# Performance work log

Hardware: AMD Instinct MI355X
Metric: run time of the kernel (lower is better)

The kernel has to match this reference:

```python
import jax, jax.numpy as jnp
import numpy as np

NEG_INF = -1e9


def setup_inputs() -> dict:
    key = jax.random.key(0)
    ks = jax.random.split(key, 12)
    B, S, D, H = 32, 2048, 512, 512
    enc_outs = jax.random.normal(ks[0], (B, S, D), dtype=jnp.float32)
    num_sent = jnp.maximum(jax.random.randint(ks[1], (B,), 0, S), 1).astype(jnp.int64)
    s = 1.0 / np.sqrt(H)
    return {
        "enc_outs": enc_outs,
        "num_sent": num_sent,
        "num_pred": 8,
        "init_h": jax.random.normal(ks[2], (1, H), dtype=jnp.float32) * s,
        "init_c": jax.random.normal(ks[3], (1, H), dtype=jnp.float32) * s,
        "init_in": jax.random.normal(ks[4], (D,), dtype=jnp.float32) * s,
        "W_ih": jax.random.uniform(ks[5], (4 * H, D), jnp.float32, -s, s),
        "W_hh": jax.random.uniform(ks[6], (4 * H, H), jnp.float32, -s, s),
        "b_ih": jax.random.uniform(ks[7], (4 * H,), jnp.float32, -s, s),
        "b_hh": jax.random.uniform(ks[8], (4 * H,), jnp.float32, -s, s),
        "attn_Wq": jax.random.uniform(ks[9], (H, D), jnp.float32, -s, s),
        "score_W": jax.random.uniform(ks[10], (1, H), jnp.float32, -s, s),
        "score_b": jax.random.uniform(ks[11], (1,), jnp.float32, -s, s),
    }


def reference(enc_outs, num_sent, num_pred, init_h, init_c, init_in,
              W_ih, W_hh, b_ih, b_hh, attn_Wq, score_W, score_b):
    B, S, D = enc_outs.shape
    H = init_h.shape[1]
    # rep_mask: True where sentence index is valid
    mask = jnp.arange(S)[None, :] < num_sent[:, None]  # [B, S]

    def lstm_cell(x, h, c):
        gates = x @ W_ih.T + b_ih + h @ W_hh.T + b_hh  # [B, 4H]
        i, f, g, o = jnp.split(gates, 4, axis=-1)
        i, f, o = jax.nn.sigmoid(i), jax.nn.sigmoid(f), jax.nn.sigmoid(o)
        c_new = f * c + i * jnp.tanh(g)
        return o * jnp.tanh(c_new), c_new

    h0 = jnp.broadcast_to(init_h[0], (B, H))
    c0 = jnp.broadcast_to(init_c[0], (B, H))
    in0 = jnp.broadcast_to(init_in, (B, D))

    def step(carry, _):
        h, c, lstm_in = carry
        h, c = lstm_cell(lstm_in, h, c)
        # glimpse attention: bilinear score, masked softmax over sentences
        q = h @ attn_Wq  # [B, D]
        logits = jnp.einsum('bd,bsd->bs', q, enc_outs)
        logits = jnp.where(mask, logits, NEG_INF)
        attn = jax.nn.softmax(logits, axis=-1)
        out = jnp.einsum('bs,bsd->bd', attn, enc_outs)  # [B, D]
        score = out @ score_W.T + score_b  # [B, 1]
        return (h, c, out), score

    _, scores = jax.lax.scan(step, (h0, c0, in0), None, length=int(num_pred))
    return scores  # [num_pred, B, 1]
```

## Files before the change

### kernel.cpp

```cpp
#include <hip/hip_runtime.h>
#include <math.h>

#define B    32
#define S    2048
#define D    512
#define H    512
#define NP   8
#define NSL  32
#define HSL  16
#define NBT  8
#define BG   4
#define NCH  8
#define SCHUNK 256

__device__ __forceinline__ float sigmoidf_(float x) {
  return 1.0f / (1.0f + __expf(-x));
}

__global__ __launch_bounds__(256)
void k_init(const float* __restrict__ W_ih, const float* __restrict__ W_hh,
            const float* __restrict__ init_h, const float* __restrict__ init_c,
            const float* __restrict__ init_in, const int* __restrict__ ns_raw,
            float4* __restrict__ Wt4, float* __restrict__ hbuf, float* __restrict__ cbuf,
            float* __restrict__ xin0, int* __restrict__ ns) {
  __shared__ float tbuf[64][65];
  const int blk = blockIdx.x, tid = threadIdx.x;
  const int jt = blk & 31, kt = blk >> 5;
  const int j0 = jt * 64, k0 = kt * 64;
  const int r0 = tid >> 6, cc = tid & 63;
  for (int rr = r0; rr < 64; rr += 4) {
    int j = j0 + rr, k = k0 + cc;
    tbuf[rr][cc] = (k < 512) ? W_ih[(size_t)j * 512 + k]
                             : W_hh[(size_t)j * 512 + (k - 512)];
  }
  __syncthreads();
  #pragma unroll
  for (int i = 0; i < 4; ++i) {
    const int kk4 = r0 * 4 + i;
    Wt4[(size_t)(kt * 16 + kk4) * 2048 + j0 + cc] =
        make_float4(tbuf[cc][kk4 * 4 + 0], tbuf[cc][kk4 * 4 + 1],
                    tbuf[cc][kk4 * 4 + 2], tbuf[cc][kk4 * 4 + 3]);
  }

  int idx = blk * 256 + tid;
  if (idx < B * H) {
    int d = idx & 511;
    hbuf[idx] = init_h[d];
    cbuf[idx] = init_c[d];
    xin0[idx] = init_in[d];
  }
  if (idx == 0) {
    bool is64 = (ns_raw[1] == 0);
    for (int i2 = 0; i2 < B; ++i2) ns[i2] = is64 ? ns_raw[2 * i2] : ns_raw[i2];
  }
}

__global__ __launch_bounds__(512, 1)
void k_step(const float* __restrict__ xin0, const float* __restrict__ bih,
            const float* __restrict__ bhh, const float* __restrict__ Wq,
            const float* __restrict__ scW, const float* __restrict__ scb,
            const float4* __restrict__ Wt4,
            const float* __restrict__ ch_m, const float* __restrict__ ch_l,
            const float* __restrict__ ch_o,
            float* __restrict__ hbuf, float* __restrict__ cbuf,
            float* __restrict__ qpart, float* __restrict__ out, int t) {
  __shared__ float X[BG][1024];
  __shared__ float gacc[8][64][5];
  __shared__ float gl[4][16][BG];
  __shared__ float hl[BG][16];
  __shared__ float sred[8][BG];

  const int tid = threadIdx.x;
  const int sl = blockIdx.x >> 3;
  const int bg = blockIdx.x & 7;
  const int b0 = bg * BG;

  if (t == 0) {
    #pragma unroll
    for (int bl = 0; bl < BG; ++bl)
      X[bl][tid] = xin0[(b0 + bl) * 512 + tid];
  } else {
    const float swd = scW[tid];
    #pragma unroll
    for (int bl = 0; bl < BG; ++bl) {
      const int b = b0 + bl;
      float M = -1e30f;
      #pragma unroll
      for (int c = 0; c < NCH; ++c) M = fmaxf(M, ch_m[b * NCH + c]);
      float e[NCH]; float L = 0.f;
      #pragma unroll
      for (int c = 0; c < NCH; ++c) {
        e[c] = __expf(ch_m[b * NCH + c] - M);
        L += ch_l[b * NCH + c] * e[c];
      }
      float v = 0.f;
      #pragma unroll
      for (int c = 0; c < NCH; ++c)
        v += ch_o[((size_t)(b * NCH + c)) * 512 + tid] * e[c];
      v *= (1.0f / L);
      X[bl][tid] = v;
      float p = v * swd;
      #pragma unroll
      for (int off = 32; off > 0; off >>= 1) p += __shfl_xor(p, off);
      if ((tid & 63) == 0) sred[tid >> 6][bl] = p;
    }
  }
  if (t < NP) {
    const float4* hsrc = (const float4*)(hbuf + (t & 1) * (B * 512));
    int bl = tid >> 7;
    int off = tid & 127;
    float4 hv = hsrc[(b0 + bl) * 128 + off];
    *(float4*)&X[bl][512 + off * 4] = hv;
  }
  __syncthreads();

  if (t >= 1 && tid < BG) {
    float s = 0.f;
    #pragma unroll
    for (int w = 0; w < 8; ++w) s += sred[w][tid];
    if (sl == 0) out[(t - 1) * B + b0 + tid] = s + scb[0];
  }
  if (t >= NP) return;

  {
    const int jloc = tid & 63;
    const int kc = tid >> 6;
    const int gi = jloc >> 4, ho = jloc & 15;
    const int jg = gi * 512 + sl * HSL + ho;
    const int k0c = kc * 128;
    const float4* wp4 = Wt4 + (size_t)(kc * 32) * 2048 + jg;
    float acc[BG] = {0, 0, 0, 0};
    for (int kk4 = 0; kk4 < 32; kk4 += 4) {
      const float4 w0 = wp4[(size_t)(kk4 + 0) * 2048];
      const float4 w1 = wp4[(size_t)(kk4 + 1) * 2048];
      const float4 w2 = wp4[(size_t)(kk4 + 2) * 2048];
      const float4 w3 = wp4[(size_t)(kk4 + 3) * 2048];
      #pragma unroll
      for (int bl = 0; bl < BG; ++bl) {
        const float4 x0 = *(const float4*)&X[bl][k0c + kk4 * 4];
        const float4 x1 = *(const float4*)&X[bl][k0c + kk4 * 4 + 4];
        const float4 x2 = *(const float4*)&X[bl][k0c + kk4 * 4 + 8];
        const float4 x3 = *(const float4*)&X[bl][k0c + kk4 * 4 + 12];
        acc[bl] += w0.x * x0.x + w0.y * x0.y + w0.z * x0.z + w0.w * x0.w
                 + w1.x * x1.x + w1.y * x1.y + w1.z * x1.z + w1.w * x1.w
                 + w2.x * x2.x + w2.y * x2.y + w2.z * x2.z + w2.w * x2.w
                 + w3.x * x3.x + w3.y * x3.y + w3.z * x3.z + w3.w * x3.w;
      }
    }
    #pragma unroll
    for (int bl = 0; bl < BG; ++bl) gacc[kc][jloc][bl] = acc[bl];
  }
  __syncthreads();

  if (tid < 256) {
    const int bl = tid >> 6, jloc = tid & 63;
    const int gi = jloc >> 4, ho = jloc & 15;
    const int jg = gi * 512 + sl * HSL + ho;
    float g = bih[jg] + bhh[jg];
    #pragma unroll
    for (int kc = 0; kc < 8; ++kc) g += gacc[kc][jloc][bl];
    gl[gi][ho][bl] = g;
  }
  __syncthreads();

  if (tid < BG * HSL) {
    const int ho = tid & 15, bl = tid >> 4;
    const int bglob = b0 + bl, hid = sl * HSL + ho;
    float i_ = sigmoidf_(gl[0][ho][bl]);
    float f_ = sigmoidf_(gl[1][ho][bl]);
    float g_ = tanhf(gl[2][ho][bl]);
    float o_ = sigmoidf_(gl[3][ho][bl]);
    float cv = cbuf[bglob * 512 + hid];
    float cn = f_ * cv + i_ * g_;
    cbuf[bglob * 512 + hid] = cn;
    float hv = o_ * tanhf(cn);
    hbuf[((t + 1) & 1) * (B * 512) + bglob * 512 + hid] = hv;
    hl[bl][ho] = hv;
  }
  __syncthreads();

  {
    float w[HSL];
    #pragma unroll
    for (int ho = 0; ho < HSL; ++ho)
      w[ho] = Wq[(size_t)(sl * HSL + ho) * 512 + tid];
    #pragma unroll
    for (int bl = 0; bl < BG; ++bl) {
      float acc = 0.f;
      #pragma unroll
      for (int ho = 0; ho < HSL; ++ho) acc += hl[bl][ho] * w[ho];
      qpart[((size_t)sl * B + b0 + bl) * 512 + tid] = acc;
    }
  }
}

__global__ __launch_bounds__(512, 1)
void k_attn(const float* __restrict__ enc, const float* __restrict__ qpart,
            const int* __restrict__ ns_buf, float* __restrict__ ch_m,
            float* __restrict__ ch_l, float* __restrict__ ch_o) {
  __shared__ float q_lds[512];
  __shared__ float wm[8], wl[8];
  __shared__ float wo[8][512];
  const int b  = blockIdx.x >> 3;
  const int ch = blockIdx.x & 7;
  const int tid = threadIdx.x;
  const int lane = tid & 63;
  const int wv = tid >> 6;

  {
    float s = 0.f;
    #pragma unroll 8
    for (int sl = 0; sl < NSL; ++sl)
      s += qpart[((size_t)sl * B + b) * 512 + tid];
    q_lds[tid] = s;
  }
  __syncthreads();

  const float4 qa  = *(const float4*)&q_lds[lane * 8];
  const float4 qb4 = *(const float4*)&q_lds[lane * 8 + 4];

  const int s0 = ch * SCHUNK;
  const int nsb = ns_buf[b];
  float m = -1e30f, l = 0.f;
  float o0=0,o1=0,o2=0,o3=0,o4=0,o5=0,o6=0,o7=0;

  const int send = min(s0 + SCHUNK, nsb);
  const size_t rowbase = (size_t)b * S;

  int r = s0 + 2 * wv;
  if (r < send) {
    bool has1 = (r + 1 < send);
    const float4* p0 = (const float4*)(enc + (rowbase + r) * 512 + lane * 8);
    const float4* p1 = (const float4*)(enc + (rowbase + (has1 ? r + 1 : r)) * 512 + lane * 8);
    float4 a0 = p0[0], a1 = p0[1];
    float4 c0 = p1[0], c1 = p1[1];
    while (true) {
      const int rn = r + 16;
      const bool hasn = (rn < send);
      float4 na0, na1, nc0, nc1;
      bool nhas1 = false;
      if (hasn) {
        nhas1 = (rn + 1 < send);
        const float4* f0 = (const float4*)(enc + (rowbase + rn) * 512 + lane * 8);
        const float4* f1 = (const float4*)(enc + (rowbase + (nhas1 ? rn + 1 : rn)) * 512 + lane * 8);
        na0 = f0[0]; na1 = f0[1]; nc0 = f1[0]; nc1 = f1[1];
      }
      float d0 = qa.x*a0.x + qa.y*a0.y + qa.z*a0.z + qa.w*a0.w
               + qb4.x*a1.x + qb4.y*a1.y + qb4.z*a1.z + qb4.w*a1.w;
      float d1 = qa.x*c0.x + qa.y*c0.y + qa.z*c0.z + qa.w*c0.w
               + qb4.x*c1.x + qb4.y*c1.y + qb4.z*c1.z + qb4.w*c1.w;
      #pragma unroll
      for (int off = 32; off > 0; off >>= 1) {
        d0 += __shfl_xor(d0, off);
        d1 += __shfl_xor(d1, off);
      }
      if (!has1) d1 = -1e30f;
      float nm = fmaxf(m, fmaxf(d0, d1));
      float sc = __expf(m - nm);
      float w0 = __expf(d0 - nm);
      float w1 = __expf(d1 - nm);
      l = l * sc + w0 + w1;
      o0 = o0*sc + w0*a0.x + w1*c0.x; o1 = o1*sc + w0*a0.y + w1*c0.y;
      o2 = o2*sc + w0*a0.z + w1*c0.z; o3 = o3*sc + w0*a0.w + w1*c0.w;
      o4 = o4*sc + w0*a1.x + w1*c1.x; o5 = o5*sc + w0*a1.y + w1*c1.y;
      o6 = o6*sc + w0*a1.z + w1*c1.z; o7 = o7*sc + w0*a1.w + w1*c1.w;
      m = nm;
      if (!hasn) break;
      r = rn; has1 = nhas1;
      a0 = na0; a1 = na1; c0 = nc0; c1 = nc1;
    }
  }
  if (lane == 0) { wm[wv] = m; wl[wv] = l; }
  float4* wop = (float4*)&wo[wv][lane * 8];
  wop[0] = make_float4(o0, o1, o2, o3);
  wop[1] = make_float4(o4, o5, o6, o7);
  __syncthreads();

  float M = wm[0];
  #pragma unroll
  for (int w = 1; w < 8; ++w) M = fmaxf(M, wm[w]);
  float e[8]; float L = 0.f;
  #pragma unroll
  for (int w = 0; w < 8; ++w) { e[w] = __expf(wm[w] - M); L += wl[w] * e[w]; }
  if (tid == 0) { ch_m[b * NCH + ch] = M; ch_l[b * NCH + ch] = L; }
  float v = 0.f;
  #pragma unroll
  for (int w = 0; w < 8; ++w) v += wo[w][tid] * e[w];
  ch_o[((size_t)(b * NCH + ch)) * 512 + tid] = v;
}

extern "C" void kernel_launch(void* const* d_in, const int* in_sizes, int n_in,
                              void* d_out, int out_size, void* d_ws, size_t ws_size,
                              hipStream_t stream) {
  const float* enc     = (const float*)d_in[0];
  const int*   ns_raw  = (const int*)d_in[1];
  const float* init_h  = (const float*)d_in[3];
  const float* init_c  = (const float*)d_in[4];
  const float* init_in = (const float*)d_in[5];
  const float* W_ih    = (const float*)d_in[6];
  const float* W_hh    = (const float*)d_in[7];
  const float* b_ih    = (const float*)d_in[8];
  const float* b_hh    = (const float*)d_in[9];
  const float* Wq      = (const float*)d_in[10];
  const float* score_W = (const float*)d_in[11];
  const float* score_b = (const float*)d_in[12];
  float* out = (float*)d_out;

  float* ws    = (float*)d_ws;
  float4* Wt4  = (float4*)ws;
  float* hbuf  = ws + 2097152;
  float* cbuf  = ws + 2129920;
  float* xin0  = ws + 2146304;
  float* qpart = ws + 2162688;
  float* ch_m  = ws + 2686976;
  float* ch_l  = ws + 2687232;
  float* ch_o  = ws + 2687488;
  int*   ns    = (int*)(ws + 2818560);

  k_init<<<512, 256, 0, stream>>>(W_ih, W_hh, init_h, init_c, init_in, ns_raw,
                                  Wt4, hbuf, cbuf, xin0, ns);
  for (int t = 0; t < NP; ++t) {
    k_step<<<NSL * NBT, 512, 0, stream>>>(xin0, b_ih, b_hh, Wq, score_W, score_b, Wt4,
                                          ch_m, ch_l, ch_o, hbuf, cbuf, qpart, out, t);
    k_attn<<<B * NCH, 512, 0, stream>>>(enc, qpart, ns, ch_m, ch_l, ch_o);
  }
  k_step<<<NSL * NBT, 512, 0, stream>>>(xin0, b_ih, b_hh, Wq, score_W, score_b, Wt4,
                                        ch_m, ch_l, ch_o, hbuf, cbuf, qpart, out, NP);
}
```

Measured before the change: 286.4 us.

## Balance attention work by splitting sequences into length-proportional chunks

```diff
diff --git a/kernel.cpp b/kernel.cpp
--- a/kernel.cpp
+++ b/kernel.cpp
@@ -10,8 +10,7 @@
 #define HSL  16
 #define NBT  8
 #define BG   4
-#define NCH  8
-#define SCHUNK 256
+#define MAXCH 256
 
 __device__ __forceinline__ float sigmoidf_(float x) {
   return 1.0f / (1.0f + __expf(-x));
@@ -22,7 +21,9 @@
             const float* __restrict__ init_h, const float* __restrict__ init_c,
             const float* __restrict__ init_in, const int* __restrict__ ns_raw,
             float4* __restrict__ Wt4, float* __restrict__ hbuf, float* __restrict__ cbuf,
-            float* __restrict__ xin0, int* __restrict__ ns) {
+            float* __restrict__ xin0, int* __restrict__ ns,
+            int* __restrict__ chunk_tab, int* __restrict__ chunk_base,
+            int* __restrict__ nchunkA, int* __restrict__ rpcA, int* __restrict__ ctot_g) {
   __shared__ float tbuf[64][65];
   const int blk = blockIdx.x, tid = threadIdx.x;
   const int jt = blk & 31, kt = blk >> 5;
@@ -51,7 +52,23 @@
   }
   if (idx == 0) {
     bool is64 = (ns_raw[1] == 0);
-    for (int i2 = 0; i2 < B; ++i2) ns[i2] = is64 ? ns_raw[2 * i2] : ns_raw[i2];
+    int total = 0;
+    for (int i2 = 0; i2 < B; ++i2) {
+      int v = is64 ? ns_raw[2 * i2] : ns_raw[i2];
+      ns[i2] = v; total += v;
+    }
+    int cidx = 0;
+    for (int b2 = 0; b2 < B; ++b2) {
+      int nch = (224 * ns[b2]) / total;
+      if (nch < 1) nch = 1;
+      int rpc = (ns[b2] + nch - 1) / nch;
+      nch = (ns[b2] + rpc - 1) / rpc;
+      chunk_base[b2] = cidx;
+      nchunkA[b2] = nch;
+      rpcA[b2] = rpc;
+      for (int c = 0; c < nch; ++c) chunk_tab[cidx++] = (b2 << 16) | c;
+    }
+    ctot_g[0] = cidx;
   }
 }
 
@@ -62,6 +79,7 @@
             const float4* __restrict__ Wt4,
             const float* __restrict__ ch_m, const float* __restrict__ ch_l,
             const float* __restrict__ ch_o,
+            const int* __restrict__ chunk_base, const int* __restrict__ nchunkA,
             float* __restrict__ hbuf, float* __restrict__ cbuf,
             float* __restrict__ qpart, float* __restrict__ out, int t) {
   __shared__ float X[BG][1024];
@@ -84,19 +102,15 @@
     #pragma unroll
     for (int bl = 0; bl < BG; ++bl) {
       const int b = b0 + bl;
+      const int cb = chunk_base[b], nc = nchunkA[b];
       float M = -1e30f;
-      #pragma unroll
-      for (int c = 0; c < NCH; ++c) M = fmaxf(M, ch_m[b * NCH + c]);
-      float e[NCH]; float L = 0.f;
-      #pragma unroll
-      for (int c = 0; c < NCH; ++c) {
-        e[c] = __expf(ch_m[b * NCH + c] - M);
-        L += ch_l[b * NCH + c] * e[c];
+      for (int c = 0; c < nc; ++c) M = fmaxf(M, ch_m[cb + c]);
+      float L = 0.f, v = 0.f;
+      for (int c = 0; c < nc; ++c) {
+        float e = __expf(ch_m[cb + c] - M);
+        L += ch_l[cb + c] * e;
+        v += ch_o[((size_t)(cb + c)) * 512 + tid] * e;
       }
-      float v = 0.f;
-      #pragma unroll
-      for (int c = 0; c < NCH; ++c)
-        v += ch_o[((size_t)(b * NCH + c)) * 512 + tid] * e[c];
       v *= (1.0f / L);
       X[bl][tid] = v;
       float p = v * swd;
@@ -196,97 +210,104 @@
 
 __global__ __launch_bounds__(512, 1)
 void k_attn(const float* __restrict__ enc, const float* __restrict__ qpart,
-            const int* __restrict__ ns_buf, float* __restrict__ ch_m,
-            float* __restrict__ ch_l, float* __restrict__ ch_o) {
+            const int* __restrict__ ns_buf, const int* __restrict__ chunk_tab,
+            const int* __restrict__ rpcA, const int* __restrict__ ctot_g,
+            float* __restrict__ ch_m, float* __restrict__ ch_l,
+            float* __restrict__ ch_o) {
   __shared__ float q_lds[512];
   __shared__ float wm[8], wl[8];
   __shared__ float wo[8][512];
-  const int b  = blockIdx.x >> 3;
-  const int ch = blockIdx.x & 7;
   const int tid = threadIdx.x;
   const int lane = tid & 63;
   const int wv = tid >> 6;
-
-  {
-    float s = 0.f;
-    #pragma unroll 8
-    for (int sl = 0; sl < NSL; ++sl)
-      s += qpart[((size_t)sl * B + b) * 512 + tid];
-    q_lds[tid] = s;
-  }
-  __syncthreads();
-
-  const float4 qa  = *(const float4*)&q_lds[lane * 8];
-  const float4 qb4 = *(const float4*)&q_lds[lane * 8 + 4];
-
-  const int s0 = ch * SCHUNK;
-  const int nsb = ns_buf[b];
-  float m = -1e30f, l = 0.f;
-  float o0=0,o1=0,o2=0,o3=0,o4=0,o5=0,o6=0,o7=0;
-
-  const int send = min(s0 + SCHUNK, nsb);
-  const size_t rowbase = (size_t)b * S;
-
-  int r = s0 + 2 * wv;
-  if (r < send) {
-    bool has1 = (r + 1 < send);
-    const float4* p0 = (const float4*)(enc + (rowbase + r) * 512 + lane * 8);
-    const float4* p1 = (const float4*)(enc + (rowbase + (has1 ? r + 1 : r)) * 512 + lane * 8);
-    float4 a0 = p0[0], a1 = p0[1];
-    float4 c0 = p1[0], c1 = p1[1];
-    while (true) {
-      const int rn = r + 16;
-      const bool hasn = (rn < send);
-      float4 na0, na1, nc0, nc1;
-      bool nhas1 = false;
-      if (hasn) {
-        nhas1 = (rn + 1 < send);
-        const float4* f0 = (const float4*)(enc + (rowbase + rn) * 512 + lane * 8);
-        const float4* f1 = (const float4*)(enc + (rowbase + (nhas1 ? rn + 1 : rn)) * 512 + lane * 8);
-        na0 = f0[0]; na1 = f0[1]; nc0 = f1[0]; nc1 = f1[1];
+  const int ctot = ctot_g[0];
+
+  for (int ci = blockIdx.x; ci < ctot; ci += 256) {
+    const int ent = chunk_tab[ci];
+    const int b = ent >> 16, c = ent & 0xffff;
+    const int rpc = rpcA[b];
+    const int s0 = c * rpc;
+    const int send = min(s0 + rpc, ns_buf[b]);
+
+    __syncthreads();
+
+    {
+      float s = 0.f;
+      #pragma unroll 8
+      for (int sl = 0; sl < NSL; ++sl)
+        s += qpart[((size_t)sl * B + b) * 512 + tid];
+      q_lds[tid] = s;
+    }
+    __syncthreads();
+
+    const float4 qa  = *(const float4*)&q_lds[lane * 8];
+    const float4 qb4 = *(const float4*)&q_lds[lane * 8 + 4];
+
+    float m = -1e30f, l = 0.f;
+    float o0=0,o1=0,o2=0,o3=0,o4=0,o5=0,o6=0,o7=0;
+    const size_t rowbase = (size_t)b * S;
+
+    int r = s0 + 2 * wv;
+    if (r < send) {
+      bool has1 = (r + 1 < send);
+      const float4* p0 = (const float4*)(enc + (rowbase + r) * 512 + lane * 8);
+      const float4* p1 = (const float4*)(enc + (rowbase + (has1 ? r + 1 : r)) * 512 + lane * 8);
+      float4 a0 = p0[0], a1 = p0[1];
+      float4 c0 = p1[0], c1 = p1[1];
+      while (true) {
+        const int rn = r + 16;
+        const bool hasn = (rn < send);
+        float4 na0, na1, nc0, nc1;
+        bool nhas1 = false;
+        if (hasn) {
+          nhas1 = (rn + 1 < send);
+          const float4* f0 = (const float4*)(enc + (rowbase + rn) * 512 + lane * 8);
+          const float4* f1 = (const float4*)(enc + (rowbase + (nhas1 ? rn + 1 : rn)) * 512 + lane * 8);
+          na0 = f0[0]; na1 = f0[1]; nc0 = f1[0]; nc1 = f1[1];
+        }
+        float d0 = qa.x*a0.x + qa.y*a0.y + qa.z*a0.z + qa.w*a0.w
+                 + qb4.x*a1.x + qb4.y*a1.y + qb4.z*a1.z + qb4.w*a1.w;
+        float d1 = qa.x*c0.x + qa.y*c0.y + qa.z*c0.z + qa.w*c0.w
+                 + qb4.x*c1.x + qb4.y*c1.y + qb4.z*c1.z + qb4.w*c1.w;
+        #pragma unroll
+        for (int off = 32; off > 0; off >>= 1) {
+          d0 += __shfl_xor(d0, off);
+          d1 += __shfl_xor(d1, off);
+        }
+        if (!has1) d1 = -1e30f;
+        float nm = fmaxf(m, fmaxf(d0, d1));
+        float sc = __expf(m - nm);
+        float w0 = __expf(d0 - nm);
+        float w1 = __expf(d1 - nm);
+        l = l * sc + w0 + w1;
+        o0 = o0*sc + w0*a0.x + w1*c0.x; o1 = o1*sc + w0*a0.y + w1*c0.y;
+        o2 = o2*sc + w0*a0.z + w1*c0.z; o3 = o3*sc + w0*a0.w + w1*c0.w;
+        o4 = o4*sc + w0*a1.x + w1*c1.x; o5 = o5*sc + w0*a1.y + w1*c1.y;
+        o6 = o6*sc + w0*a1.z + w1*c1.z; o7 = o7*sc + w0*a1.w + w1*c1.w;
+        m = nm;
+        if (!hasn) break;
+        r = rn; has1 = nhas1;
+        a0 = na0; a1 = na1; c0 = nc0; c1 = nc1;
       }
-      float d0 = qa.x*a0.x + qa.y*a0.y + qa.z*a0.z + qa.w*a0.w
-               + qb4.x*a1.x + qb4.y*a1.y + qb4.z*a1.z + qb4.w*a1.w;
-      float d1 = qa.x*c0.x + qa.y*c0.y + qa.z*c0.z + qa.w*c0.w
-               + qb4.x*c1.x + qb4.y*c1.y + qb4.z*c1.z + qb4.w*c1.w;
-      #pragma unroll
-      for (int off = 32; off > 0; off >>= 1) {
-        d0 += __shfl_xor(d0, off);
-        d1 += __shfl_xor(d1, off);
-      }
-      if (!has1) d1 = -1e30f;
-      float nm = fmaxf(m, fmaxf(d0, d1));
-      float sc = __expf(m - nm);
-      float w0 = __expf(d0 - nm);
-      float w1 = __expf(d1 - nm);
-      l = l * sc + w0 + w1;
-      o0 = o0*sc + w0*a0.x + w1*c0.x; o1 = o1*sc + w0*a0.y + w1*c0.y;
-      o2 = o2*sc + w0*a0.z + w1*c0.z; o3 = o3*sc + w0*a0.w + w1*c0.w;
-      o4 = o4*sc + w0*a1.x + w1*c1.x; o5 = o5*sc + w0*a1.y + w1*c1.y;
-      o6 = o6*sc + w0*a1.z + w1*c1.z; o7 = o7*sc + w0*a1.w + w1*c1.w;
-      m = nm;
-      if (!hasn) break;
-      r = rn; has1 = nhas1;
-      a0 = na0; a1 = na1; c0 = nc0; c1 = nc1;
-    }
-  }
-  if (lane == 0) { wm[wv] = m; wl[wv] = l; }
-  float4* wop = (float4*)&wo[wv][lane * 8];
-  wop[0] = make_float4(o0, o1, o2, o3);
-  wop[1] = make_float4(o4, o5, o6, o7);
-  __syncthreads();
-
-  float M = wm[0];
-  #pragma unroll
-  for (int w = 1; w < 8; ++w) M = fmaxf(M, wm[w]);
-  float e[8]; float L = 0.f;
-  #pragma unroll
-  for (int w = 0; w < 8; ++w) { e[w] = __expf(wm[w] - M); L += wl[w] * e[w]; }
-  if (tid == 0) { ch_m[b * NCH + ch] = M; ch_l[b * NCH + ch] = L; }
-  float v = 0.f;
-  #pragma unroll
-  for (int w = 0; w < 8; ++w) v += wo[w][tid] * e[w];
-  ch_o[((size_t)(b * NCH + ch)) * 512 + tid] = v;
+    }
+    if (lane == 0) { wm[wv] = m; wl[wv] = l; }
+    float4* wop = (float4*)&wo[wv][lane * 8];
+    wop[0] = make_float4(o0, o1, o2, o3);
+    wop[1] = make_float4(o4, o5, o6, o7);
+    __syncthreads();
+
+    float M = wm[0];
+    #pragma unroll
+    for (int w = 1; w < 8; ++w) M = fmaxf(M, wm[w]);
+    float e[8]; float L = 0.f;
+    #pragma unroll
+    for (int w = 0; w < 8; ++w) { e[w] = __expf(wm[w] - M); L += wl[w] * e[w]; }
+    if (tid == 0) { ch_m[ci] = M; ch_l[ci] = L; }
+    float v = 0.f;
+    #pragma unroll
+    for (int w = 0; w < 8; ++w) v += wo[w][tid] * e[w];
+    ch_o[((size_t)ci) * 512 + tid] = v;
+  }
 }
 
 extern "C" void kernel_launch(void* const* d_in, const int* in_sizes, int n_in,
@@ -315,15 +336,24 @@
   float* ch_m  = ws + 2686976;
   float* ch_l  = ws + 2687232;
   float* ch_o  = ws + 2687488;
-  int*   ns    = (int*)(ws + 2818560);
+  int*   ns         = (int*)(ws + 2818560);
+  int*   chunk_tab  = (int*)(ws + 2818592);
+  int*   chunk_base = (int*)(ws + 2818848);
+  int*   nchunkA    = (int*)(ws + 2818880);
+  int*   rpcA       = (int*)(ws + 2818912);
+  int*   ctot_g     = (int*)(ws + 2818944);
 
   k_init<<<512, 256, 0, stream>>>(W_ih, W_hh, init_h, init_c, init_in, ns_raw,
-                                  Wt4, hbuf, cbuf, xin0, ns);
+                                  Wt4, hbuf, cbuf, xin0, ns,
+                                  chunk_tab, chunk_base, nchunkA, rpcA, ctot_g);
   for (int t = 0; t < NP; ++t) {
     k_step<<<NSL * NBT, 512, 0, stream>>>(xin0, b_ih, b_hh, Wq, score_W, score_b, Wt4,
-                                          ch_m, ch_l, ch_o, hbuf, cbuf, qpart, out, t);
-    k_attn<<<B * NCH, 512, 0, stream>>>(enc, qpart, ns, ch_m, ch_l, ch_o);
+                                          ch_m, ch_l, ch_o, chunk_base, nchunkA,
+                                          hbuf, cbuf, qpart, out, t);
+    k_attn<<<256, 512, 0, stream>>>(enc, qpart, ns, chunk_tab, rpcA, ctot_g,
+                                    ch_m, ch_l, ch_o);
   }
   k_step<<<NSL * NBT, 512, 0, stream>>>(xin0, b_ih, b_hh, Wq, score_W, score_b, Wt4,
-                                        ch_m, ch_l, ch_o, hbuf, cbuf, qpart, out, NP);
-}
+                                        ch_m, ch_l, ch_o, chunk_base, nchunkA,
+                                        hbuf, cbuf, qpart, out, NP);
+}
```

Measured after the change: 385.7 us. 34.7% more time.
